# Optimization experiments

Measured on AMD Instinct MI355X. Metric: run time of the kernel, lower is better.

Reference implementation:

```python
import jax, jax.numpy as jnp
import numpy as np

N = 100_000      # nodes
E = 3_200_000    # edges (avg degree 32)
G = 512          # graphs in batch
IN_DIM = 3
H = 64
L = 3
BN_EPS = 1e-5


def setup_inputs() -> dict:
    key = jax.random.key(0)
    ks = jax.random.split(key, 14)
    s = 0.1
    x = jax.random.normal(ks[0], (N, IN_DIM), jnp.float32)
    edge_index = jax.random.randint(ks[1], (2, E), 0, N, dtype=jnp.int32)
    batch = jnp.sort(jax.random.randint(ks[2], (N,), 0, G, dtype=jnp.int32))
    # GIN MLP params per layer: Linear(in,H) -> ReLU -> Linear(H,H)
    w1_0 = jax.random.normal(ks[3], (IN_DIM, H), jnp.float32) * s   # layer 0 first linear
    w1_r = jax.random.normal(ks[4], (L - 1, H, H), jnp.float32) * s  # layers 1..L-1 first linear
    b1 = jax.random.normal(ks[5], (L, H), jnp.float32) * s
    w2 = jax.random.normal(ks[6], (L, H, H), jnp.float32) * s
    b2 = jax.random.normal(ks[7], (L, H), jnp.float32) * s
    gamma = 1.0 + jax.random.normal(ks[8], (L, H), jnp.float32) * 0.05
    beta = jax.random.normal(ks[9], (L, H), jnp.float32) * 0.05
    wout = jax.random.normal(ks[10], (H, H), jnp.float32) * s
    bout = jax.random.normal(ks[11], (H,), jnp.float32) * s
    return {"x": x, "edge_index": edge_index, "batch": batch,
            "w1_0": w1_0, "w1_r": w1_r, "b1": b1, "w2": w2, "b2": b2,
            "gamma": gamma, "beta": beta, "wout": wout, "bout": bout}


def reference(x, edge_index, batch, w1_0, w1_r, b1, w2, b2, gamma, beta, wout, bout):
    src, dst = edge_index[0], edge_index[1]
    for i in range(L):
        # GINConv: h = mlp((1+eps)*x + sum_{j in N(i)} x_j), eps = 0
        agg = jax.ops.segment_sum(x[src], dst, num_segments=N)  # [N, d]
        h = x + agg
        W1 = w1_0 if i == 0 else w1_r[i - 1]
        h = jax.nn.relu(h @ W1 + b1[i]) @ w2[i] + b2[i]          # [N, H]
        # BatchNorm1d (training mode: biased batch stats over nodes)
        mu = h.mean(axis=0)
        var = h.var(axis=0)
        h = (h - mu) / jnp.sqrt(var + BN_EPS) * gamma[i] + beta[i]
        x = jax.nn.relu(h)
    # global_mean_pool: segment mean over graph ids
    sums = jax.ops.segment_sum(x, batch, num_segments=G)                        # [G, H]
    cnt = jax.ops.segment_sum(jnp.ones((N, 1), x.dtype), batch, num_segments=G)  # [G, 1]
    graph_repr = jnp.where(cnt > 0, sums / jnp.maximum(cnt, 1.0), 0.0)
    return graph_repr @ wout + bout  # [G, H]
```

## Files before the change

kernel.cpp:

```cpp
#include <hip/hip_runtime.h>


#define NBMAX 1024
#define CAP 4608
#define CHUNK 8192
#define NBLK_MAX 512
#define MSTR 72

typedef __attribute__((ext_vector_type(8))) short bf16x8;
typedef __attribute__((ext_vector_type(4))) float f32x4;

static __device__ __forceinline__ bf16x8 as_bf16x8(uint4 u) {
    union { uint4 a; bf16x8 b; } x; x.a = u; return x.b;
}
static __device__ __forceinline__ unsigned short bf16r(float v) {
    unsigned u = __float_as_uint(v);
    return (unsigned short)((u + 0x7FFFu + ((u >> 16) & 1u)) >> 16);
}
static __device__ __forceinline__ unsigned bf16pack2(float a, float b) {
    return (unsigned)bf16r(a) | ((unsigned)bf16r(b) << 16);
}

__global__ void prep_weights(const float* __restrict__ w1_0, const float* __restrict__ w1_r,
                             const float* __restrict__ w2, unsigned short* __restrict__ w1T0,
                             unsigned short* __restrict__ w1T, unsigned short* __restrict__ w2T) {
    int t = blockIdx.x * 256 + threadIdx.x;
    if (t < 64 * 32) {
        int c = t >> 5, k = t & 31;
        w1T0[t] = bf16r(k < 3 ? w1_0[k * 64 + c] : 0.f);
    }
    if (t < 2 * 64 * 64) {
        int l = t >> 12, r = t & 4095, c = r >> 6, k = r & 63;
        w1T[t] = bf16r(w1_r[l * 4096 + k * 64 + c]);
    }
    if (t < 3 * 64 * 64) {
        int l = t >> 12, r = t & 4095, c = r >> 6, k = r & 63;
        w2T[t] = bf16r(w2[l * 4096 + k * 64 + c]);
    }
}

__global__ __launch_bounds__(512) void scatter_sort(
    const int* __restrict__ src, const int* __restrict__ dst,
    int* __restrict__ bucketed2, int* __restrict__ offsTab, int E) {
    __shared__ int hist[NBMAX];
    __shared__ int offs[NBMAX];
    __shared__ int stage[CHUNK];
    __shared__ int wsum8[8];
    int t = threadIdx.x, blk = blockIdx.x;
    int e0 = blk * CHUNK, e1 = min(e0 + CHUNK, E);
    int len = e1 - e0;
    hist[t] = 0; hist[t + 512] = 0;
    __syncthreads();
    for (int e = e0 + t; e < e1; e += 512) atomicAdd(&hist[dst[e] >> 7], 1);
    __syncthreads();
    int h0 = hist[2 * t], h1 = hist[2 * t + 1];
    int pair = h0 + h1;
    int lane = t & 63;
    int incl = pair;
#pragma unroll
    for (int d = 1; d < 64; d <<= 1) {
        int up = __shfl_up(incl, d);
        if (lane >= d) incl += up;
    }
    if (lane == 63) wsum8[t >> 6] = incl;
    __syncthreads();
    int wid = t >> 6, wpre = 0;
    for (int i = 0; i < wid; i++) wpre += wsum8[i];
    int exclP = wpre + incl - pair;
    offs[2 * t] = exclP;
    offs[2 * t + 1] = exclP + h0;
    hist[2 * t] = 0; hist[2 * t + 1] = 0;
    __syncthreads();
    offsTab[blk * 1025 + t] = offs[t];
    offsTab[blk * 1025 + t + 512] = offs[t + 512];
    if (t == 0) offsTab[blk * 1025 + 1024] = len;
    for (int e = e0 + t; e < e1; e += 512) {
        int d = dst[e];
        int bk = d >> 7;
        int r = offs[bk] + atomicAdd(&hist[bk], 1);
        stage[r] = src[e] | ((d & 127) << 20);
    }
    __syncthreads();
    for (int j = t; j < len; j += 512) bucketed2[e0 + j] = stage[j];
}

__global__ __launch_bounds__(256) void bucket_csr(
    const int* __restrict__ bucketed2, const int* __restrict__ offsTab,
    int* __restrict__ csrOut, int* __restrict__ rowstart, int* __restrict__ rowend,
    int N, int nblk) {
    __shared__ int ein[CAP];
    __shared__ int emid[CAP];
    __shared__ int runs[NBLK_MAX];
    __shared__ int rbeg[NBLK_MAX];
    __shared__ int hist[128];
    __shared__ int base[129];
    __shared__ int wsum4[4];
    __shared__ int wtot2[2];
    int b = blockIdx.x, t = threadIdx.x, node0 = b << 7;
    for (int r = t; r < NBLK_MAX; r += 256) {
        int l = 0, g0 = 0;
        if (r < nblk) {
            int beg = offsTab[r * 1025 + b];
            int end = offsTab[r * 1025 + b + 1];
            l = end - beg;
            g0 = r * CHUNK + beg;
        }
        runs[r] = l;
        rbeg[r] = g0;
    }
    __syncthreads();
    {
        int l0 = runs[2 * t], l1 = runs[2 * t + 1];
        int pair = l0 + l1;
        int lane = t & 63;
        int incl = pair;
#pragma unroll
        for (int d = 1; d < 64; d <<= 1) {
            int up = __shfl_up(incl, d);
            if (lane >= d) incl += up;
        }
        if (lane == 63) wsum4[t >> 6] = incl;
        __syncthreads();
        int wid = t >> 6, wpre = 0;
        for (int i = 0; i < wid; i++) wpre += wsum4[i];
        int exclP = wpre + incl - pair;
        runs[2 * t] = exclP + l0;
        runs[2 * t + 1] = exclP + l0 + l1;
    }
    __syncthreads();
    int cnt = min(runs[NBLK_MAX - 1], CAP);
    for (int j = t; j < cnt; j += 256) {
        int lo = 0, hi = nblk - 1;
        while (lo < hi) {
            int m = (lo + hi) >> 1;
            if (runs[m] > j) hi = m; else lo = m + 1;
        }
        int st = lo ? runs[lo - 1] : 0;
        ein[j] = bucketed2[rbeg[lo] + (j - st)];
    }
    if (t < 128) hist[t] = 0;
    __syncthreads();
    for (int j = t; j < cnt; j += 256) atomicAdd(&hist[(ein[j] & 0xFFFFF) >> 10], 1);
    __syncthreads();
    {
        int lane = t & 63;
        int hv = (t < 128) ? hist[t] : 0;
        int incl = hv;
#pragma unroll
        for (int d = 1; d < 64; d <<= 1) {
            int up = __shfl_up(incl, d);
            if (lane >= d) incl += up;
        }
        if (t < 128 && lane == 63) wtot2[t >> 6] = incl;
        __syncthreads();
        if (t >= 64 && t < 128) incl += wtot2[0];
        if (t < 128) { base[t + 1] = incl; hist[t] = 0; }
        if (t == 0) base[0] = 0;
    }
    __syncthreads();
    for (int j = t; j < cnt; j += 256) {
        int p = ein[j];
        int sb = (p & 0xFFFFF) >> 10;
        int pos = base[sb] + atomicAdd(&hist[sb], 1);
        emid[pos] = p;
    }
    __syncthreads();
    if (t < 128) hist[t] = 0;
    __syncthreads();
    for (int j = t; j < cnt; j += 256) atomicAdd(&hist[emid[j] >> 20], 1);
    __syncthreads();
    {
        int lane = t & 63;
        int hv = (t < 128) ? hist[t] : 0;
        int incl = hv;
#pragma unroll
        for (int d = 1; d < 64; d <<= 1) {
            int up = __shfl_up(incl, d);
            if (lane >= d) incl += up;
        }
        if (t < 128 && lane == 63) wtot2[t >> 6] = incl;
        __syncthreads();
        if (t >= 64 && t < 128) incl += wtot2[0];
        if (t < 128) { base[t + 1] = incl; hist[t] = 0; }
        if (t == 0) base[0] = 0;
    }
    __syncthreads();
    if (t < 128) {
        int n = node0 + t;
        if (n < N) {
            rowstart[n] = b * CAP + base[t];
            rowend[n] = b * CAP + base[t + 1];
        }
    }
    __syncthreads();
    for (int j = t; j < cnt; j += 256) {
        int p = emid[j];
        int local = p >> 20;
        int pos = base[local] + atomicAdd(&hist[local], 1);
        ein[pos] = p & 0xFFFFF;
    }
    __syncthreads();
    for (int j = t; j < cnt; j += 256) csrOut[b * CAP + j] = ein[j];
}

__device__ __forceinline__ void accum_bf16(const uint4 u,
                                           const float4 scA, const float4 scB,
                                           const float4 shA, const float4 shB,
                                           float* __restrict__ a) {
    a[0] += fmaxf(__uint_as_float(u.x << 16) * scA.x + shA.x, 0.f);
    a[1] += fmaxf(__uint_as_float(u.x & 0xFFFF0000u) * scA.y + shA.y, 0.f);
    a[2] += fmaxf(__uint_as_float(u.y << 16) * scA.z + shA.z, 0.f);
    a[3] += fmaxf(__uint_as_float(u.y & 0xFFFF0000u) * scA.w + shA.w, 0.f);
    a[4] += fmaxf(__uint_as_float(u.z << 16) * scB.x + shB.x, 0.f);
    a[5] += fmaxf(__uint_as_float(u.z & 0xFFFF0000u) * scB.y + shB.y, 0.f);
    a[6] += fmaxf(__uint_as_float(u.w << 16) * scB.z + shB.z, 0.f);
    a[7] += fmaxf(__uint_as_float(u.w & 0xFFFF0000u) * scB.w + shB.w, 0.f);
}

template <bool L0>
__global__ __launch_bounds__(256) void gin_layer(
    const void* __restrict__ actInRaw,
    const int* __restrict__ rowstart, const int* __restrict__ rowend,
    const int* __restrict__ csr,
    const float* __restrict__ bnsumPrev, const float* __restrict__ bnsqPrev,
    const float* __restrict__ gammaPrev, const float* __restrict__ betaPrev,
    const uint4* __restrict__ w1Tu, const float* __restrict__ b1,
    const uint4* __restrict__ w2Tu, const float* __restrict__ b2,
    uint4* __restrict__ houtU4,
    float* __restrict__ partS, float* __restrict__ partQ, int N) {
    __shared__ __align__(16) unsigned short acts[32 * MSTR];
    __shared__ __align__(16) unsigned short mids[32 * MSTR];
    __shared__ float red[8][64];
    __shared__ float scs[64], shs[64];
    int t = threadIdx.x;
    int tileBase = blockIdx.x * 32;
    uint4* actsU4 = (uint4*)acts;
    const uint4* midU4 = (const uint4*)mids;
    const uint4 z4 = make_uint4(0, 0, 0, 0);

    if (!L0) {
        if (t < 64) {
            float mu = bnsumPrev[t] / (float)N;
            float var = bnsqPrev[t] / (float)N - mu * mu;
            float s = gammaPrev[t] * rsqrtf(var + 1e-5f);
            scs[t] = s;
            shs[t] = betaPrev[t] - mu * s;
        }
        __syncthreads();
    }

    if (L0) {
        const float* x = (const float*)actInRaw;
        int ni = t & 31, seg = t >> 5;
        int n = tileBase + ni;
        float s0 = 0.f, s1 = 0.f, s2 = 0.f;
        if (n < N) {
            int srow = rowstart[n], erow = rowend[n];
            for (int j = srow + seg; j < erow; j += 8) {
                int nb = csr[j];
                s0 += x[nb * 3]; s1 += x[nb * 3 + 1]; s2 += x[nb * 3 + 2];
            }
            if (seg == 0) { s0 += x[n * 3]; s1 += x[n * 3 + 1]; s2 += x[n * 3 + 2]; }
        }
        float* stg = (float*)mids;
        stg[seg * 96 + ni * 3 + 0] = s0;
        stg[seg * 96 + ni * 3 + 1] = s1;
        stg[seg * 96 + ni * 3 + 2] = s2;
        __syncthreads();
        if (t < 32) {
            float a0 = 0.f, a1 = 0.f, a2 = 0.f;
#pragma unroll
            for (int g2 = 0; g2 < 8; g2++) {
                a0 += stg[g2 * 96 + t * 3 + 0];
                a1 += stg[g2 * 96 + t * 3 + 1];
                a2 += stg[g2 * 96 + t * 3 + 2];
            }
            actsU4[t * 9] = make_uint4(bf16pack2(a0, a1), bf16pack2(a2, 0.f), 0u, 0u);
        }
    } else {
        const uint4* hr = (const uint4*)actInRaw;
        int ni = t >> 3, l = t & 7;
        int n = tileBase + ni;
        int c0i = l * 8;
        float4 scA = *(const float4*)&scs[c0i], scB = *(const float4*)&scs[c0i + 4];
        float4 shA = *(const float4*)&shs[c0i], shB = *(const float4*)&shs[c0i + 4];
        float A[8] = {0,0,0,0,0,0,0,0};
        float B[8] = {0,0,0,0,0,0,0,0};
        if (n < N) {
            accum_bf16(hr[(size_t)n * 8 + l], scA, scB, shA, shB, A);
            int s = rowstart[n], e = rowend[n];
            int j = s;
            for (; j + 3 < e; j += 4) {
                int i0 = csr[j], i1 = csr[j + 1], i2 = csr[j + 2], i3 = csr[j + 3];
                uint4 w0 = hr[(size_t)i0 * 8 + l];
                uint4 w1 = hr[(size_t)i1 * 8 + l];
                uint4 w2 = hr[(size_t)i2 * 8 + l];
                uint4 w3 = hr[(size_t)i3 * 8 + l];
                accum_bf16(w0, scA, scB, shA, shB, A);
                accum_bf16(w1, scA, scB, shA, shB, B);
                accum_bf16(w2, scA, scB, shA, shB, A);
                accum_bf16(w3, scA, scB, shA, shB, B);
            }
            for (; j < e; j++) {
                uint4 w = hr[(size_t)csr[j] * 8 + l];
                accum_bf16(w, scA, scB, shA, shB, A);
            }
        }
        uint4 o;
        o.x = bf16pack2(A[0] + B[0], A[1] + B[1]);
        o.y = bf16pack2(A[2] + B[2], A[3] + B[3]);
        o.z = bf16pack2(A[4] + B[4], A[5] + B[5]);
        o.w = bf16pack2(A[6] + B[6], A[7] + B[7]);
        actsU4[ni * 9 + l] = o;
    }

    int w = t >> 6, l64 = t & 63, m16 = l64 & 15, q = l64 >> 4;
    int col = w * 16 + m16;
    bf16x8 w1f0, w1f1, w2f0, w2f1;
    float bias1 = b1[col], bias2 = b2[col];
    if (L0) {
        w1f0 = as_bf16x8(w1Tu[col * 4 + q]);
    } else {
        w1f0 = as_bf16x8(w1Tu[col * 8 + q]);
        w1f1 = as_bf16x8(w1Tu[col * 8 + 4 + q]);
    }
    w2f0 = as_bf16x8(w2Tu[col * 8 + q]);
    w2f1 = as_bf16x8(w2Tu[col * 8 + 4 + q]);
    __syncthreads();
#pragma unroll
    for (int rg = 0; rg < 2; rg++) {
        int rloc = rg * 16 + m16;
        bf16x8 a0 = as_bf16x8(L0 ? (q == 0 ? actsU4[rloc * 9] : z4)
                                 : actsU4[rloc * 9 + q]);
        f32x4 acc = {bias1, bias1, bias1, bias1};
        if (L0) {
            acc = __builtin_amdgcn_mfma_f32_16x16x32_bf16(a0, w1f0, acc, 0, 0, 0);
        } else {
            bf16x8 a1 = as_bf16x8(actsU4[rloc * 9 + 4 + q]);
            acc = __builtin_amdgcn_mfma_f32_16x16x32_bf16(a0, w1f0, acc, 0, 0, 0);
            acc = __builtin_amdgcn_mfma_f32_16x16x32_bf16(a1, w1f1, acc, 0, 0, 0);
        }
#pragma unroll
        for (int r = 0; r < 4; r++) {
            int row = rg * 16 + q * 4 + r;
            mids[row * MSTR + col] = bf16r(fmaxf(acc[r], 0.f));
        }
    }
    __syncthreads();
    f32x4 accs[2];
#pragma unroll
    for (int rg = 0; rg < 2; rg++) {
        int rloc = rg * 16 + m16;
        bf16x8 a20 = as_bf16x8(midU4[rloc * 9 + q]);
        bf16x8 a21 = as_bf16x8(midU4[rloc * 9 + 4 + q]);
        f32x4 acc = {bias2, bias2, bias2, bias2};
        acc = __builtin_amdgcn_mfma_f32_16x16x32_bf16(a20, w2f0, acc, 0, 0, 0);
        acc = __builtin_amdgcn_mfma_f32_16x16x32_bf16(a21, w2f1, acc, 0, 0, 0);
        accs[rg] = acc;
    }
    float sA = 0.f, sB = 0.f, qA = 0.f, qB = 0.f;
#pragma unroll
    for (int rg = 0; rg < 2; rg++) {
#pragma unroll
        for (int r = 0; r < 4; r++) {
            int row = rg * 16 + q * 4 + r;
            float v = accs[rg][r];
            if (tileBase + row < N) {
                if (rg == 0) { sA += v; qA += v * v; } else { sB += v; qB += v * v; }
            }
            acts[row * MSTR + col] = bf16r(v);
        }
    }
    __syncthreads();
    {
        int row = t >> 3, qo = t & 7;
        int gr = tileBase + row;
        if (gr < N) houtU4[(size_t)gr * 8 + qo] = actsU4[row * 9 + qo];
    }
    red[q][col] = sA;
    red[4 + q][col] = sB;
    __syncthreads();
    if (t < 64) {
        float S = 0.f;
        for (int i = 0; i < 8; i++) S += red[i][t];
        partS[blockIdx.x * 64 + t] = S;
    }
    __syncthreads();
    red[q][col] = qA;
    red[4 + q][col] = qB;
    __syncthreads();
    if (t < 64) {
        float S = 0.f;
        for (int i = 0; i < 8; i++) S += red[i][t];
        partQ[blockIdx.x * 64 + t] = S;
    }
}

__global__ __launch_bounds__(256) void bn_reduce(
    const float* __restrict__ partS, const float* __restrict__ partQ,
    float* __restrict__ bnsum, float* __restrict__ bnsq, int nParts) {
    __shared__ float rs[256], rq[256];
    int b = blockIdx.x, t = threadIdx.x;
    float S = 0.f, Q = 0.f;
    for (int p = t; p < nParts; p += 256) {
        S += partS[p * 64 + b];
        Q += partQ[p * 64 + b];
    }
    rs[t] = S; rq[t] = Q;
    __syncthreads();
    for (int off = 128; off > 0; off >>= 1) {
        if (t < off) { rs[t] += rs[t + off]; rq[t] += rq[t + off]; }
        __syncthreads();
    }
    if (t == 0) { bnsum[b] = rs[0]; bnsq[b] = rq[0]; }
}

__device__ __forceinline__ int lowb(const int* __restrict__ a, int n, int v) {
    int lo = 0, hi = n;
    while (lo < hi) {
        int m = (lo + hi) >> 1;
        if (a[m] < v) lo = m + 1; else hi = m;
    }
    return lo;
}

__global__ __launch_bounds__(256) void bn_pool_out(
    const unsigned short* __restrict__ h, const int* __restrict__ batch,
    const float* __restrict__ bnsum, const float* __restrict__ bnsq,
    const float* __restrict__ gamma, const float* __restrict__ beta,
    const float* __restrict__ wout, const float* __restrict__ bout,
    float* __restrict__ out, int N) {
    __shared__ float sc[64], sh[64];
    __shared__ float part[4][64];
    __shared__ float gr[64];
    __shared__ int range[2];
    int g = blockIdx.x, t = threadIdx.x;
    if (t < 64) {
        float mu = bnsum[t] / (float)N;
        float var = bnsq[t] / (float)N - mu * mu;
        float s = gamma[t] * rsqrtf(var + 1e-5f);
        sc[t] = s;
        sh[t] = beta[t] - mu * s;
    }
    if (t == 64) range[0] = lowb(batch, N, g);
    if (t == 65) range[1] = lowb(batch, N, g + 1);
    __syncthreads();
    int s0 = range[0], s1 = range[1];
    int col = t & 63, ro = t >> 6;
    float acc = 0.f;
    for (int n = s0 + ro; n < s1; n += 4) {
        float v = __uint_as_float(((unsigned)h[(size_t)n * 64 + col]) << 16);
        acc += fmaxf(v * sc[col] + sh[col], 0.f);
    }
    part[ro][col] = acc;
    __syncthreads();
    if (t < 64) {
        float S = part[0][t] + part[1][t] + part[2][t] + part[3][t];
        float c = (float)(s1 - s0);
        gr[t] = (c > 0.f) ? S / c : 0.f;
    }
    __syncthreads();
    if (t < 64) {
        float a = bout[t];
        for (int f = 0; f < 64; f++) a += gr[f] * wout[f * 64 + t];
        out[g * 64 + t] = a;
    }
}

extern "C" void kernel_launch(void* const* d_in, const int* in_sizes, int n_in,
                              void* d_out, int out_size, void* d_ws, size_t ws_size,
                              hipStream_t stream) {
    const float* x     = (const float*)d_in[0];
    const int*   ei    = (const int*)d_in[1];
    const int*   batch = (const int*)d_in[2];
    const float* w1_0  = (const float*)d_in[3];
    const float* w1_r  = (const float*)d_in[4];
    const float* b1    = (const float*)d_in[5];
    const float* w2    = (const float*)d_in[6];
    const float* b2    = (const float*)d_in[7];
    const float* gamma = (const float*)d_in[8];
    const float* beta  = (const float*)d_in[9];
    const float* wout  = (const float*)d_in[10];
    const float* bout  = (const float*)d_in[11];
    float* out = (float*)d_out;

    const int N = in_sizes[2];
    const int E = in_sizes[1] / 2;
    const int NB = (N + 127) >> 7;
    const int nblk = (E + CHUNK - 1) / CHUNK;
    const int nT32 = (N + 31) >> 5;

    unsigned short* hbX = (unsigned short*)d_ws;
    unsigned short* hbY = hbX + (size_t)N * 64;
    int* bucketed2 = (int*)(hbY + (size_t)N * 64);
    int* offsTab   = bucketed2 + (size_t)nblk * CHUNK;
    int* csrOut    = offsTab + (size_t)nblk * 1025;
    int* rowstart  = csrOut + (size_t)NB * CAP;
    int* rowend    = rowstart + N;
    float* bnstats = (float*)(rowend + N);
    float* partS   = bnstats + 384;
    float* partQ   = partS + (size_t)nT32 * 64;
    unsigned short* w1T0 = (unsigned short*)(partQ + (size_t)nT32 * 64);
    unsigned short* w1T  = w1T0 + 64 * 32;
    unsigned short* w2T  = w1T + 2 * 64 * 64;

    const int* srcv = ei;
    const int* dstv = ei + E;

    prep_weights<<<48, 256, 0, stream>>>(w1_0, w1_r, w2, w1T0, w1T, w2T);

    scatter_sort<<<nblk, 512, 0, stream>>>(srcv, dstv, bucketed2, offsTab, E);
    bucket_csr<<<NB, 256, 0, stream>>>(bucketed2, offsTab, csrOut, rowstart, rowend, N, nblk);

    gin_layer<true><<<nT32, 256, 0, stream>>>(x, rowstart, rowend, csrOut,
                                              nullptr, nullptr, nullptr, nullptr,
                                              (const uint4*)w1T0, b1,
                                              (const uint4*)w2T, b2,
                                              (uint4*)hbX, partS, partQ, N);
    bn_reduce<<<64, 256, 0, stream>>>(partS, partQ, bnstats, bnstats + 64, nT32);

    gin_layer<false><<<nT32, 256, 0, stream>>>(hbX, rowstart, rowend, csrOut,
                                               bnstats, bnstats + 64, gamma, beta,
                                               (const uint4*)w1T, b1 + 64,
                                               (const uint4*)(w2T + 4096), b2 + 64,
                                               (uint4*)hbY, partS, partQ, N);
    bn_reduce<<<64, 256, 0, stream>>>(partS, partQ, bnstats + 128, bnstats + 192, nT32);

    gin_layer<false><<<nT32, 256, 0, stream>>>(hbY, rowstart, rowend, csrOut,
                                               bnstats + 128, bnstats + 192,
                                               gamma + 64, beta + 64,
                                               (const uint4*)(w1T + 4096), b1 + 128,
                                               (const uint4*)(w2T + 8192), b2 + 128,
                                               (uint4*)hbX, partS, partQ, N);
    bn_reduce<<<64, 256, 0, stream>>>(partS, partQ, bnstats + 256, bnstats + 320, nT32);

    bn_pool_out<<<512, 256, 0, stream>>>(hbX, batch, bnstats + 256, bnstats + 320,
                                         gamma + 128, beta + 128, wout, bout, out, N);
}
```

Measured before the change: 345.4 us.

## Fold weight prep into scatter kernel, unroll gather by 8, vectorize pool

Weight transposition and bf16 conversion move into an extra block of the scatter_sort launch, which removes one kernel launch. The neighbor gather loop in gin_layer gains an 8-wide unrolled stage so more independent loads are in flight per thread. The final pooling kernel now reads 16-byte vectors with 32 row groups per block instead of scalar bf16 loads, at the cost of a larger shared-memory reduction.

```diff
diff --git a/kernel.cpp b/kernel.cpp
--- a/kernel.cpp
+++ b/kernel.cpp
@@ -21,32 +21,32 @@
     return (unsigned)bf16r(a) | ((unsigned)bf16r(b) << 16);
 }
 
-__global__ void prep_weights(const float* __restrict__ w1_0, const float* __restrict__ w1_r,
-                             const float* __restrict__ w2, unsigned short* __restrict__ w1T0,
-                             unsigned short* __restrict__ w1T, unsigned short* __restrict__ w2T) {
-    int t = blockIdx.x * 256 + threadIdx.x;
-    if (t < 64 * 32) {
-        int c = t >> 5, k = t & 31;
-        w1T0[t] = bf16r(k < 3 ? w1_0[k * 64 + c] : 0.f);
-    }
-    if (t < 2 * 64 * 64) {
-        int l = t >> 12, r = t & 4095, c = r >> 6, k = r & 63;
-        w1T[t] = bf16r(w1_r[l * 4096 + k * 64 + c]);
-    }
-    if (t < 3 * 64 * 64) {
-        int l = t >> 12, r = t & 4095, c = r >> 6, k = r & 63;
-        w2T[t] = bf16r(w2[l * 4096 + k * 64 + c]);
-    }
-}
-
 __global__ __launch_bounds__(512) void scatter_sort(
     const int* __restrict__ src, const int* __restrict__ dst,
-    int* __restrict__ bucketed2, int* __restrict__ offsTab, int E) {
+    int* __restrict__ bucketed2, int* __restrict__ offsTab, int E, int nblk,
+    const float* __restrict__ w1_0, const float* __restrict__ w1_r,
+    const float* __restrict__ w2, unsigned short* __restrict__ w1T0,
+    unsigned short* __restrict__ w1T, unsigned short* __restrict__ w2T) {
+    int t = threadIdx.x, blk = blockIdx.x;
+    if (blk >= nblk) {
+        for (int i = t; i < 64 * 32; i += 512) {
+            int c = i >> 5, k = i & 31;
+            w1T0[i] = bf16r(k < 3 ? w1_0[k * 64 + c] : 0.f);
+        }
+        for (int i = t; i < 2 * 64 * 64; i += 512) {
+            int l = i >> 12, r = i & 4095, c = r >> 6, k = r & 63;
+            w1T[i] = bf16r(w1_r[l * 4096 + k * 64 + c]);
+        }
+        for (int i = t; i < 3 * 64 * 64; i += 512) {
+            int l = i >> 12, r = i & 4095, c = r >> 6, k = r & 63;
+            w2T[i] = bf16r(w2[l * 4096 + k * 64 + c]);
+        }
+        return;
+    }
     __shared__ int hist[NBMAX];
     __shared__ int offs[NBMAX];
     __shared__ int stage[CHUNK];
     __shared__ int wsum8[8];
-    int t = threadIdx.x, blk = blockIdx.x;
     int e0 = blk * CHUNK, e1 = min(e0 + CHUNK, E);
     int len = e1 - e0;
     hist[t] = 0; hist[t + 512] = 0;
@@ -290,6 +290,26 @@
             accum_bf16(hr[(size_t)n * 8 + l], scA, scB, shA, shB, A);
             int s = rowstart[n], e = rowend[n];
             int j = s;
+            for (; j + 7 < e; j += 8) {
+                int i0 = csr[j], i1 = csr[j + 1], i2 = csr[j + 2], i3 = csr[j + 3];
+                int i4 = csr[j + 4], i5 = csr[j + 5], i6 = csr[j + 6], i7 = csr[j + 7];
+                uint4 w0 = hr[(size_t)i0 * 8 + l];
+                uint4 w1 = hr[(size_t)i1 * 8 + l];
+                uint4 w2 = hr[(size_t)i2 * 8 + l];
+                uint4 w3 = hr[(size_t)i3 * 8 + l];
+                uint4 w4 = hr[(size_t)i4 * 8 + l];
+                uint4 w5 = hr[(size_t)i5 * 8 + l];
+                uint4 w6 = hr[(size_t)i6 * 8 + l];
+                uint4 w7 = hr[(size_t)i7 * 8 + l];
+                accum_bf16(w0, scA, scB, shA, shB, A);
+                accum_bf16(w1, scA, scB, shA, shB, B);
+                accum_bf16(w2, scA, scB, shA, shB, A);
+                accum_bf16(w3, scA, scB, shA, shB, B);
+                accum_bf16(w4, scA, scB, shA, shB, A);
+                accum_bf16(w5, scA, scB, shA, shB, B);
+                accum_bf16(w6, scA, scB, shA, shB, A);
+                accum_bf16(w7, scA, scB, shA, shB, B);
+            }
             for (; j + 3 < e; j += 4) {
                 int i0 = csr[j], i1 = csr[j + 1], i2 = csr[j + 2], i3 = csr[j + 3];
                 uint4 w0 = hr[(size_t)i0 * 8 + l];
@@ -425,13 +445,13 @@
 }
 
 __global__ __launch_bounds__(256) void bn_pool_out(
-    const unsigned short* __restrict__ h, const int* __restrict__ batch,
+    const uint4* __restrict__ hr, const int* __restrict__ batch,
     const float* __restrict__ bnsum, const float* __restrict__ bnsq,
     const float* __restrict__ gamma, const float* __restrict__ beta,
     const float* __restrict__ wout, const float* __restrict__ bout,
     float* __restrict__ out, int N) {
     __shared__ float sc[64], sh[64];
-    __shared__ float part[4][64];
+    __shared__ float part[32][64];
     __shared__ float gr[64];
     __shared__ int range[2];
     int g = blockIdx.x, t = threadIdx.x;
@@ -446,16 +466,21 @@
     if (t == 65) range[1] = lowb(batch, N, g + 1);
     __syncthreads();
     int s0 = range[0], s1 = range[1];
-    int col = t & 63, ro = t >> 6;
-    float acc = 0.f;
-    for (int n = s0 + ro; n < s1; n += 4) {
-        float v = __uint_as_float(((unsigned)h[(size_t)n * 64 + col]) << 16);
-        acc += fmaxf(v * sc[col] + sh[col], 0.f);
-    }
-    part[ro][col] = acc;
+    int o = t & 7, ro = t >> 3;
+    int c0 = o * 8;
+    float4 scA = *(const float4*)&sc[c0], scB = *(const float4*)&sc[c0 + 4];
+    float4 shA = *(const float4*)&sh[c0], shB = *(const float4*)&sh[c0 + 4];
+    float A[8] = {0,0,0,0,0,0,0,0};
+    for (int n = s0 + ro; n < s1; n += 32) {
+        uint4 u = hr[(size_t)n * 8 + o];
+        accum_bf16(u, scA, scB, shA, shB, A);
+    }
+#pragma unroll
+    for (int k = 0; k < 8; k++) part[ro][c0 + k] = A[k];
     __syncthreads();
     if (t < 64) {
-        float S = part[0][t] + part[1][t] + part[2][t] + part[3][t];
+        float S = 0.f;
+        for (int i = 0; i < 32; i++) S += part[i][t];
         float c = (float)(s1 - s0);
         gr[t] = (c > 0.f) ? S / c : 0.f;
     }
@@ -507,9 +532,8 @@
     const int* srcv = ei;
     const int* dstv = ei + E;
 
-    prep_weights<<<48, 256, 0, stream>>>(w1_0, w1_r, w2, w1T0, w1T, w2T);
-
-    scatter_sort<<<nblk, 512, 0, stream>>>(srcv, dstv, bucketed2, offsTab, E);
+    scatter_sort<<<nblk + 1, 512, 0, stream>>>(srcv, dstv, bucketed2, offsTab, E, nblk,
+                                               w1_0, w1_r, w2, w1T0, w1T, w2T);
     bucket_csr<<<NB, 256, 0, stream>>>(bucketed2, offsTab, csrOut, rowstart, rowend, N, nblk);
 
     gin_layer<true><<<nT32, 256, 0, stream>>>(x, rowstart, rowend, csrOut,
@@ -534,6 +558,7 @@
                                                (uint4*)hbX, partS, partQ, N);
     bn_reduce<<<64, 256, 0, stream>>>(partS, partQ, bnstats + 256, bnstats + 320, nT32);
 
-    bn_pool_out<<<512, 256, 0, stream>>>(hbX, batch, bnstats + 256, bnstats + 320,
+    bn_pool_out<<<512, 256, 0, stream>>>((const uint4*)hbX, batch,
+                                         bnstats + 256, bnstats + 320,
                                          gamma + 128, beta + 128, wout, bout, out, N);
 }
```

Measured after the change: 348.4 us. Within noise of the previous version (+0.8%).
